# Performance work log

Measured on AMD Instinct MI355X. Metric: run time of the kernel, lower is better.

The kernel has to match this reference:

```python
import jax, jax.numpy as jnp
import numpy as np

N, FEAT, K = 131072, 64, 2048  # points, features, clusters
DECAY = 0.99


def setup_inputs() -> dict:
    key = jax.random.key(0)
    k1, k2 = jax.random.split(key)
    x = jax.random.normal(k1, (N, FEAT), dtype=jnp.float32)
    centroids = jax.random.normal(k2, (K, FEAT), dtype=jnp.float32)
    return {"x": x, "centroids": centroids}


def reference(x, centroids):
    dists = (jnp.sum(x * x, axis=-1)[:, None]
             + jnp.sum(centroids * centroids, axis=-1)[None, :]
             - 2.0 * (x @ centroids.T))
    assignments = jnp.argmin(dists, axis=-1)  # [N] int

    # index_reduce 'mean' with include_self=False: scatter-mean of x into clusters;
    # clusters receiving no points keep their old centroid.
    k = centroids.shape[0]
    sums = jax.ops.segment_sum(x, assignments, num_segments=k)          # [K, FEAT]
    counts = jax.ops.segment_sum(jnp.ones((x.shape[0],), x.dtype),
                                 assignments, num_segments=k)           # [K]
    means = sums / jnp.maximum(counts, 1.0)[:, None]
    new_centroids = jnp.where(counts[:, None] > 0, means, centroids)

    # centroids.lerp_(new_centroids, 1 - decay)
    updated = DECAY * centroids + (1.0 - DECAY) * new_centroids
    return assignments, updated
```

## Files before the change

### kernel.cpp

```cpp
#include <hip/hip_runtime.h>
#include <math.h>

#define NPTS    131072
#define FEAT    64
#define KCLUS   2048
#define CHUNKC  256
#define NCHUNK  (KCLUS / CHUNKC)
#define PPW     32
#define WPB     4
#define PPB     (PPW * WPB)
#define CANDC   10
#define CG      32

typedef __attribute__((ext_vector_type(8))) short frag_ab;
typedef __attribute__((ext_vector_type(4))) float frag_cd;

__device__ __forceinline__ short f2bf(float f) {
    unsigned u = __float_as_uint(f);
    u += 0x7FFFu + ((u >> 16) & 1u);
    return (short)(u >> 16);
}

__device__ __forceinline__ float exact_dist(const float* __restrict__ x,
                                            const float* __restrict__ c,
                                            float cnv, int p, int kk) {
    const float4* xr4 = (const float4*)&x[(size_t)p * FEAT];
    const float4* cr4 = (const float4*)&c[(size_t)kk * FEAT];
    float s = 0.f;
#pragma unroll
    for (int j = 0; j < 16; ++j) {
        float4 a4 = xr4[j], b4 = cr4[j];
        s = fmaf(a4.x, b4.x, s); s = fmaf(a4.y, b4.y, s);
        s = fmaf(a4.z, b4.z, s); s = fmaf(a4.w, b4.w, s);
    }
    return fmaf(-2.f, s, cnv);
}

__global__ void cprep_kernel(const float* __restrict__ c, float* __restrict__ cnorm,
                             short* __restrict__ cbs_t, float* __restrict__ cmax) {
    int k = blockIdx.x * blockDim.x + threadIdx.x;
    if (k >= KCLUS) return;
    const float4* row = (const float4*)&c[k * FEAT];
    float s = 0.f;
#pragma unroll
    for (int j = 0; j < 16; ++j) {
        float4 v = row[j];
        s = fmaf(v.x, v.x, s); s = fmaf(v.y, v.y, s);
        s = fmaf(v.z, v.z, s); s = fmaf(v.w, v.w, s);
        short4 b;
        b.x = f2bf(-2.f * v.x); b.y = f2bf(-2.f * v.y);
        b.z = f2bf(-2.f * v.z); b.w = f2bf(-2.f * v.w);
        *(short4*)&cbs_t[((size_t)(j >> 1) * KCLUS + k) * 8 + (j & 1) * 4] = b;
    }
    cnorm[k] = s;
    atomicMax((int*)cmax, __float_as_int(sqrtf(s)));
}

__device__ __forceinline__ void load_chunk(const short* __restrict__ cbs_t,
                                           const float* __restrict__ cnorm,
                                           int k0, int tid,
                                           frag_ab pre[8], float* cnpre) {
#pragma unroll
    for (int p8 = 0; p8 < 8; ++p8)
        pre[p8] = *(const frag_ab*)&cbs_t[((size_t)p8 * KCLUS + k0 + tid) * 8];
    *cnpre = cnorm[k0 + tid];
}

__global__ __launch_bounds__(256) void assign_kernel(
    const float* __restrict__ x, const float* __restrict__ c,
    const short* __restrict__ cbs_t, const float* __restrict__ cnorm,
    const float* __restrict__ cmaxp,
    float* __restrict__ out_assign, unsigned short* __restrict__ a16)
{
    __shared__ short csh[8 * CHUNKC * 8];
    __shared__ float cnsh[CHUNKC];

    const int tid = threadIdx.x, wv = tid >> 6, lane = tid & 63;
    const int col = lane & 15, q = lane >> 4;
    const int pt0 = blockIdx.x * PPB + wv * PPW;

    frag_ab A[2][2];
    float nrm[2];
#pragma unroll
    for (int rt = 0; rt < 2; ++rt) {
        float ps = 0.f;
#pragma unroll
        for (int kh = 0; kh < 2; ++kh) {
            const float4* xp = (const float4*)&x[(size_t)(pt0 + rt * 16 + col) * FEAT + kh * 32 + q * 8];
            float4 v0 = xp[0], v1 = xp[1];
            frag_ab a;
            a[0] = f2bf(v0.x); a[1] = f2bf(v0.y); a[2] = f2bf(v0.z); a[3] = f2bf(v0.w);
            a[4] = f2bf(v1.x); a[5] = f2bf(v1.y); a[6] = f2bf(v1.z); a[7] = f2bf(v1.w);
            A[rt][kh] = a;
            ps = fmaf(v0.x, v0.x, ps); ps = fmaf(v0.y, v0.y, ps);
            ps = fmaf(v0.z, v0.z, ps); ps = fmaf(v0.w, v0.w, ps);
            ps = fmaf(v1.x, v1.x, ps); ps = fmaf(v1.y, v1.y, ps);
            ps = fmaf(v1.z, v1.z, ps); ps = fmaf(v1.w, v1.w, ps);
        }
        ps += __shfl_xor(ps, 16);
        ps += __shfl_xor(ps, 32);
        nrm[rt] = sqrtf(ps);
    }

    float m[2][4];
#pragma unroll
    for (int rt = 0; rt < 2; ++rt)
#pragma unroll
        for (int r = 0; r < 4; ++r) m[rt][r] = INFINITY;

    frag_ab pre[8];
    float   cnpre;

    load_chunk(cbs_t, cnorm, 0, tid, pre, &cnpre);
    for (int c8 = 0; c8 < NCHUNK; ++c8) {
        __syncthreads();
#pragma unroll
        for (int p8 = 0; p8 < 8; ++p8)
            *(frag_ab*)&csh[(p8 * CHUNKC + tid) * 8] = pre[p8];
        cnsh[tid] = cnpre;
        __syncthreads();
        if (c8 < NCHUNK - 1)
            load_chunk(cbs_t, cnorm, (c8 + 1) * CHUNKC, tid, pre, &cnpre);

#pragma unroll 4
        for (int ct = 0; ct < CHUNKC / 16; ++ct) {
            const int lc = ct * 16 + col;
            frag_ab b0 = *(const frag_ab*)&csh[(q * CHUNKC + lc) * 8];
            frag_ab b1 = *(const frag_ab*)&csh[((4 + q) * CHUNKC + lc) * 8];
            const float cnv = cnsh[lc];
#pragma unroll
            for (int rt = 0; rt < 2; ++rt) {
                frag_cd acc = {cnv, cnv, cnv, cnv};
                acc = __builtin_amdgcn_mfma_f32_16x16x32_bf16(A[rt][0], b0, acc, 0, 0, 0);
                acc = __builtin_amdgcn_mfma_f32_16x16x32_bf16(A[rt][1], b1, acc, 0, 0, 0);
                m[rt][0] = fminf(m[rt][0], acc[0]);
                m[rt][1] = fminf(m[rt][1], acc[1]);
                m[rt][2] = fminf(m[rt][2], acc[2]);
                m[rt][3] = fminf(m[rt][3], acc[3]);
            }
        }
    }

    const float cmax = *cmaxp;
    float t[2][4];
#pragma unroll
    for (int rt = 0; rt < 2; ++rt)
#pragma unroll
        for (int r = 0; r < 4; ++r) {
            float mm = m[rt][r];
            mm = fminf(mm, __shfl_xor(mm, 1));
            mm = fminf(mm, __shfl_xor(mm, 2));
            mm = fminf(mm, __shfl_xor(mm, 4));
            mm = fminf(mm, __shfl_xor(mm, 8));
            float xnp = __shfl(nrm[rt], q * 4 + r);
            t[rt][r] = mm + 0.034f * xnp * cmax;
        }

    unsigned codes[CANDC];
    int ccnt = 0;

    load_chunk(cbs_t, cnorm, 0, tid, pre, &cnpre);
    for (int c8 = 0; c8 < NCHUNK; ++c8) {
        __syncthreads();
#pragma unroll
        for (int p8 = 0; p8 < 8; ++p8)
            *(frag_ab*)&csh[(p8 * CHUNKC + tid) * 8] = pre[p8];
        cnsh[tid] = cnpre;
        __syncthreads();
        if (c8 < NCHUNK - 1)
            load_chunk(cbs_t, cnorm, (c8 + 1) * CHUNKC, tid, pre, &cnpre);

        const int k0 = c8 * CHUNKC;
#pragma unroll 2
        for (int ct = 0; ct < CHUNKC / 16; ++ct) {
            const int lc = ct * 16 + col;
            frag_ab b0 = *(const frag_ab*)&csh[(q * CHUNKC + lc) * 8];
            frag_ab b1 = *(const frag_ab*)&csh[((4 + q) * CHUNKC + lc) * 8];
            const float cnv = cnsh[lc];
            const int kk = k0 + lc;
#pragma unroll
            for (int rt = 0; rt < 2; ++rt) {
                frag_cd acc = {cnv, cnv, cnv, cnv};
                acc = __builtin_amdgcn_mfma_f32_16x16x32_bf16(A[rt][0], b0, acc, 0, 0, 0);
                acc = __builtin_amdgcn_mfma_f32_16x16x32_bf16(A[rt][1], b1, acc, 0, 0, 0);
#pragma unroll
                for (int r = 0; r < 4; ++r) {
                    if (acc[r] <= t[rt][r]) {
                        unsigned code = ((unsigned)(rt * 16 + q * 4 + r) << 11) | (unsigned)kk;
#pragma unroll
                        for (int s = 0; s < CANDC; ++s)
                            if (s == ccnt) codes[s] = code;
                        ccnt++;
                    }
                }
            }
        }
    }

    const bool anyovf = __any(ccnt > CANDC);

    if (!anyovf) {
        float bestd[2][4];
        int   bestk[2][4];
#pragma unroll
        for (int rt = 0; rt < 2; ++rt)
#pragma unroll
            for (int r = 0; r < 4; ++r) { bestd[rt][r] = INFINITY; bestk[rt][r] = 0x7fffffff; }

        for (int i = 0; i < CANDC; ++i) {
            if (i < ccnt) {
                unsigned code = codes[i];
                int pl = (int)(code >> 11), kk = (int)(code & 2047u);
                float e = exact_dist(x, c, cnorm[kk], pt0 + pl, kk);
                int crt = pl >> 4, cr = pl & 3;
#pragma unroll
                for (int rt = 0; rt < 2; ++rt)
#pragma unroll
                    for (int r = 0; r < 4; ++r)
                        if (crt == rt && cr == r &&
                            (e < bestd[rt][r] || (e == bestd[rt][r] && kk < bestk[rt][r]))) {
                            bestd[rt][r] = e; bestk[rt][r] = kk;
                        }
            }
        }

#pragma unroll
        for (int rt = 0; rt < 2; ++rt) {
#pragma unroll
            for (int r = 0; r < 4; ++r) {
                float bd = bestd[rt][r]; int bk = bestk[rt][r];
#pragma unroll
                for (int mask = 1; mask <= 8; mask <<= 1) {
                    float od = __shfl_xor(bd, mask);
                    int   ok = __shfl_xor(bk, mask);
                    if (od < bd || (od == bd && ok < bk)) { bd = od; bk = ok; }
                }
                bestd[rt][r] = bd; bestk[rt][r] = bk;
            }
            if (col == 0) {
                float4 w = { (float)bestk[rt][0], (float)bestk[rt][1],
                             (float)bestk[rt][2], (float)bestk[rt][3] };
                *(float4*)&out_assign[pt0 + rt * 16 + q * 4] = w;
                ushort4 u = { (unsigned short)bestk[rt][0], (unsigned short)bestk[rt][1],
                              (unsigned short)bestk[rt][2], (unsigned short)bestk[rt][3] };
                *(ushort4*)&a16[pt0 + rt * 16 + q * 4] = u;
            }
        }
    } else {
        for (int pp = 0; pp < PPW; ++pp) {
            const int p = pt0 + pp;
            float bd = INFINITY; int bk = 0x7fffffff;
            for (int kk = lane; kk < KCLUS; kk += 64) {
                float e = exact_dist(x, c, cnorm[kk], p, kk);
                if (e < bd || (e == bd && kk < bk)) { bd = e; bk = kk; }
            }
#pragma unroll
            for (int mask = 1; mask <= 32; mask <<= 1) {
                float od = __shfl_xor(bd, mask);
                int   ok = __shfl_xor(bk, mask);
                if (od < bd || (od == bd && ok < bk)) { bd = od; bk = ok; }
            }
            if (lane == 0) {
                out_assign[p] = (float)bk;
                a16[p] = (unsigned short)bk;
            }
        }
    }
}

__global__ void scatter_kernel(const float* __restrict__ x,
                               const unsigned short* __restrict__ a16,
                               float* __restrict__ sums, int* __restrict__ counts) {
    __shared__ float wsum[4][CG][64];
    __shared__ int   wcnt[4][CG];

    const int tid = threadIdx.x, wv = tid >> 6, lane = tid & 63;
    const int c0 = blockIdx.x * CG;

    for (int idx = tid; idx < 4 * CG * 64; idx += 256) ((float*)wsum)[idx] = 0.f;
    if (tid < 4 * CG) ((int*)wcnt)[tid] = 0;
    __syncthreads();

    const int base = blockIdx.y * 16384 + wv * 4096;
#pragma unroll 1
    for (int it = 0; it < 64; ++it) {
        const int pbase = base + it * 64;
        int a = (int)a16[pbase + lane];
        unsigned long long mask = __ballot(a >= c0 && a < c0 + CG);
        while (mask) {
            int j = __ffsll((long long)mask) - 1;
            mask &= mask - 1;
            int cl = __shfl(a, j) - c0;
            float xv = x[(size_t)(pbase + j) * FEAT + lane];
            wsum[wv][cl][lane] += xv;
            if (lane == 0) wcnt[wv][cl] += 1;
        }
    }
    __syncthreads();

    for (int idx = tid; idx < CG * 64; idx += 256) {
        int cl = idx >> 6, ln = idx & 63;
        float s = wsum[0][cl][ln] + wsum[1][cl][ln] + wsum[2][cl][ln] + wsum[3][cl][ln];
        atomicAdd(&sums[(size_t)(c0 + cl) * FEAT + ln], s);
    }
    if (tid < CG) {
        int cc = wcnt[0][tid] + wcnt[1][tid] + wcnt[2][tid] + wcnt[3][tid];
        if (cc) atomicAdd(&counts[c0 + tid], cc);
    }
}

__global__ void update_kernel(const float* __restrict__ c,
                              const float* __restrict__ sums,
                              const int* __restrict__ counts,
                              float* __restrict__ out_upd) {
    int i = blockIdx.x * blockDim.x + threadIdx.x;
    if (i < KCLUS * FEAT) {
        int   k   = i >> 6;
        float cv  = c[i];
        int   cnt = counts[k];
        float nc  = (cnt > 0) ? (sums[i] / (float)cnt) : cv;
        out_upd[i] = 0.99f * cv + 0.01f * nc;
    }
}

extern "C" void kernel_launch(void* const* d_in, const int* in_sizes, int n_in,
                              void* d_out, int out_size, void* d_ws, size_t ws_size,
                              hipStream_t stream) {
    const float* x = (const float*)d_in[0];
    const float* c = (const float*)d_in[1];

    float* out        = (float*)d_out;
    float* out_assign = out;
    float* out_upd    = out + NPTS;

    char* ws = (char*)d_ws;
    constexpr size_t O_CNORM = 0;
    constexpr size_t O_CBS   = 8192;
    constexpr size_t O_ZERO  = 8192 + 262144;
    constexpr size_t O_CMAX  = O_ZERO;
    constexpr size_t O_SUMS  = O_ZERO + 64;
    constexpr size_t O_CNTS  = O_SUMS + 524288;
    constexpr size_t ZERO_LEN = 64 + 524288 + 8192;
    constexpr size_t O_A16   = O_ZERO + ZERO_LEN;

    float*    cnorm  = (float*)(ws + O_CNORM);
    short*    cbs_t  = (short*)(ws + O_CBS);
    float*    cmax   = (float*)(ws + O_CMAX);
    float*    sums   = (float*)(ws + O_SUMS);
    int*      counts = (int*)(ws + O_CNTS);
    unsigned short* a16 = (unsigned short*)(ws + O_A16);

    hipMemsetAsync(ws + O_ZERO, 0, ZERO_LEN, stream);

    cprep_kernel<<<KCLUS / 64, 64, 0, stream>>>(c, cnorm, cbs_t, cmax);
    assign_kernel<<<NPTS / PPB, 256, 0, stream>>>(x, c, cbs_t, cnorm, cmax,
                                                  out_assign, a16);
    scatter_kernel<<<dim3(KCLUS / CG, 8), 256, 0, stream>>>(x, a16, sums, counts);
    update_kernel<<<(KCLUS * FEAT) / 256, 256, 0, stream>>>(c, sums, counts, out_upd);
}
```

Measured before the change: 248.2 us.

## Fold memset into cprep, recompute cmax per wave, fuse update into scatter

Zeroing of sums, counts and tickets moves into the centroid-prep kernel, so the separate memset launch goes away. The global atomicMax for the max centroid norm is dropped; each assign wave instead reduces all 2048 centroid norms itself. The update kernel is folded into the scatter kernel through a per-cluster-group ticket counter, so the last of the 8 y-blocks writes the lerped centroids. This trades two launches for extra per-wave norm reads and a threadfence/atomic handshake at the end of each scatter block.

```diff
diff --git a/kernel.cpp b/kernel.cpp
--- a/kernel.cpp
+++ b/kernel.cpp
@@ -37,9 +37,19 @@
 }
 
 __global__ void cprep_kernel(const float* __restrict__ c, float* __restrict__ cnorm,
-                             short* __restrict__ cbs_t, float* __restrict__ cmax) {
+                             short* __restrict__ cbs_t,
+                             float* __restrict__ sums, int* __restrict__ counts,
+                             int* __restrict__ tickets) {
     int k = blockIdx.x * blockDim.x + threadIdx.x;
     if (k >= KCLUS) return;
+
+    float4 z = {0.f, 0.f, 0.f, 0.f};
+    float4* srow = (float4*)&sums[(size_t)k * FEAT];
+#pragma unroll
+    for (int j = 0; j < FEAT / 4; ++j) srow[j] = z;
+    counts[k] = 0;
+    if (k < 16) tickets[k] = 0;
+
     const float4* row = (const float4*)&c[k * FEAT];
     float s = 0.f;
 #pragma unroll
@@ -53,7 +63,6 @@
         *(short4*)&cbs_t[((size_t)(j >> 1) * KCLUS + k) * 8 + (j & 1) * 4] = b;
     }
     cnorm[k] = s;
-    atomicMax((int*)cmax, __float_as_int(sqrtf(s)));
 }
 
 __device__ __forceinline__ void load_chunk(const short* __restrict__ cbs_t,
@@ -69,7 +78,6 @@
 __global__ __launch_bounds__(256) void assign_kernel(
     const float* __restrict__ x, const float* __restrict__ c,
     const short* __restrict__ cbs_t, const float* __restrict__ cnorm,
-    const float* __restrict__ cmaxp,
     float* __restrict__ out_assign, unsigned short* __restrict__ a16)
 {
     __shared__ short csh[8 * CHUNKC * 8];
@@ -141,7 +149,15 @@
         }
     }
 
-    const float cmax = *cmaxp;
+    float cmv = 0.f;
+#pragma unroll
+    for (int j = 0; j < KCLUS / 64; ++j)
+        cmv = fmaxf(cmv, cnorm[j * 64 + lane]);
+#pragma unroll
+    for (int mask = 1; mask <= 32; mask <<= 1)
+        cmv = fmaxf(cmv, __shfl_xor(cmv, mask));
+    const float cmax = sqrtf(cmv);
+
     float t[2][4];
 #pragma unroll
     for (int rt = 0; rt < 2; ++rt)
@@ -270,12 +286,17 @@
 
 __global__ void scatter_kernel(const float* __restrict__ x,
                                const unsigned short* __restrict__ a16,
-                               float* __restrict__ sums, int* __restrict__ counts) {
+                               const float* __restrict__ c,
+                               float* __restrict__ sums, int* __restrict__ counts,
+                               int* __restrict__ tickets,
+                               float* __restrict__ out_upd) {
     __shared__ float wsum[4][CG][64];
     __shared__ int   wcnt[4][CG];
+    __shared__ int   lastFlag;
 
     const int tid = threadIdx.x, wv = tid >> 6, lane = tid & 63;
-    const int c0 = blockIdx.x * CG;
+    const int cg = blockIdx.x;
+    const int c0 = cg * CG;
 
     for (int idx = tid; idx < 4 * CG * 64; idx += 256) ((float*)wsum)[idx] = 0.f;
     if (tid < 4 * CG) ((int*)wcnt)[tid] = 0;
@@ -307,19 +328,29 @@
         int cc = wcnt[0][tid] + wcnt[1][tid] + wcnt[2][tid] + wcnt[3][tid];
         if (cc) atomicAdd(&counts[c0 + tid], cc);
     }
-}
-
-__global__ void update_kernel(const float* __restrict__ c,
-                              const float* __restrict__ sums,
-                              const int* __restrict__ counts,
-                              float* __restrict__ out_upd) {
-    int i = blockIdx.x * blockDim.x + threadIdx.x;
-    if (i < KCLUS * FEAT) {
-        int   k   = i >> 6;
-        float cv  = c[i];
-        int   cnt = counts[k];
-        float nc  = (cnt > 0) ? (sums[i] / (float)cnt) : cv;
-        out_upd[i] = 0.99f * cv + 0.01f * nc;
+
+    __threadfence();
+    __syncthreads();
+    if (tid == 0) {
+        const int word = cg >> 2, sh = (cg & 3) * 8;
+        int old = __hip_atomic_fetch_add(&tickets[word], 1 << sh,
+                                         __ATOMIC_ACQ_REL, __HIP_MEMORY_SCOPE_AGENT);
+        lastFlag = (((old >> sh) & 0xff) == 7);
+    }
+    __syncthreads();
+    if (lastFlag) {
+        __threadfence();
+        for (int idx = tid; idx < CG * FEAT; idx += 256) {
+            int gi = c0 * FEAT + idx;
+            int gk = c0 + (idx >> 6);
+            float s = __hip_atomic_load(&sums[gi], __ATOMIC_RELAXED,
+                                        __HIP_MEMORY_SCOPE_AGENT);
+            int cnt = __hip_atomic_load(&counts[gk], __ATOMIC_RELAXED,
+                                        __HIP_MEMORY_SCOPE_AGENT);
+            float cv = c[gi];
+            float nc = (cnt > 0) ? (s / (float)cnt) : cv;
+            out_upd[gi] = 0.99f * cv + 0.01f * nc;
+        }
     }
 }
 
@@ -336,25 +367,23 @@
     char* ws = (char*)d_ws;
     constexpr size_t O_CNORM = 0;
     constexpr size_t O_CBS   = 8192;
-    constexpr size_t O_ZERO  = 8192 + 262144;
-    constexpr size_t O_CMAX  = O_ZERO;
-    constexpr size_t O_SUMS  = O_ZERO + 64;
+    constexpr size_t O_TICK  = 8192 + 262144;
+    constexpr size_t O_SUMS  = O_TICK + 64;
     constexpr size_t O_CNTS  = O_SUMS + 524288;
-    constexpr size_t ZERO_LEN = 64 + 524288 + 8192;
-    constexpr size_t O_A16   = O_ZERO + ZERO_LEN;
+    constexpr size_t O_A16   = O_CNTS + 8192;
 
     float*    cnorm  = (float*)(ws + O_CNORM);
     short*    cbs_t  = (short*)(ws + O_CBS);
-    float*    cmax   = (float*)(ws + O_CMAX);
+    int*      tickets= (int*)(ws + O_TICK);
     float*    sums   = (float*)(ws + O_SUMS);
     int*      counts = (int*)(ws + O_CNTS);
     unsigned short* a16 = (unsigned short*)(ws + O_A16);
 
-    hipMemsetAsync(ws + O_ZERO, 0, ZERO_LEN, stream);
-
-    cprep_kernel<<<KCLUS / 64, 64, 0, stream>>>(c, cnorm, cbs_t, cmax);
-    assign_kernel<<<NPTS / PPB, 256, 0, stream>>>(x, c, cbs_t, cnorm, cmax,
+    cprep_kernel<<<KCLUS / 64, 64, 0, stream>>>(c, cnorm, cbs_t,
+                                                sums, counts, tickets);
+    assign_kernel<<<NPTS / PPB, 256, 0, stream>>>(x, c, cbs_t, cnorm,
                                                   out_assign, a16);
-    scatter_kernel<<<dim3(KCLUS / CG, 8), 256, 0, stream>>>(x, a16, sums, counts);
-    update_kernel<<<(KCLUS * FEAT) / 256, 256, 0, stream>>>(c, sums, counts, out_upd);
-}
+    scatter_kernel<<<dim3(KCLUS / CG, 8), 256, 0, stream>>>(x, a16, c, sums,
+                                                            counts, tickets,
+                                                            out_upd);
+}
```

Result: slower. 335.1 us (+35.0%).
